# Optimization experiments

Hardware: AMD Instinct MI355X
Metric: run time of the kernel (lower is better)

## Reference

```python
import jax, jax.numpy as jnp
import numpy as np

DIM = 256
N_HEADS = 4
B, N = 2, 4096


def setup_inputs() -> dict:
    key = jax.random.key(0)
    ks = jax.random.split(key, 10)
    s = DIM ** -0.5
    return {
        "x": jax.random.normal(ks[0], (B, N, DIM), dtype=jnp.float32),
        "q_w": jax.random.normal(ks[1], (DIM, DIM), dtype=jnp.float32) * s,
        "q_b": jnp.zeros((DIM,), dtype=jnp.float32),
        "k_w": jax.random.normal(ks[2], (DIM, DIM), dtype=jnp.float32) * s,
        "k_b": jnp.zeros((DIM,), dtype=jnp.float32),
        "v_w": jax.random.normal(ks[3], (DIM, DIM), dtype=jnp.float32) * s,
        "v_b": jnp.zeros((DIM,), dtype=jnp.float32),
        "o_w": jax.random.normal(ks[4], (DIM, DIM), dtype=jnp.float32) * s,
        "o_b": jnp.zeros((DIM,), dtype=jnp.float32),
        "tau": jnp.ones((1,), dtype=jnp.float32),
    }


def reference(x, q_w, q_b, k_w, k_b, v_w, v_b, o_w, o_b, tau):
    Bsz, Nlen, C = x.shape
    H = N_HEADS
    Dh = C // H
    scale = C ** -0.5  # source uses full dim, not head_dim
    Q = (x @ q_w.T + q_b).reshape(Bsz, Nlen, H, Dh)
    K = (x @ k_w.T + k_b).reshape(Bsz, Nlen, H, Dh)
    V = (x @ v_w.T + v_b).reshape(Bsz, Nlen, H, Dh)
    attn = jnp.einsum('bnhd,bmhd->bhnm', Q, K) * scale
    # soft-threshold gate: keep only |attn| > tau, then relu
    attn = jax.nn.relu(jnp.where(jnp.abs(attn) > tau, attn, 0.0))
    attn = jax.nn.softmax(attn, axis=-1)
    out = jnp.einsum('bhnm,bmhd->bnhd', attn, V).reshape(Bsz, Nlen, C)
    return out @ o_w.T + o_b
```

## Files before the change

### kernel.cpp

```cpp
#include <hip/hip_runtime.h>

#define SEQ   4096
#define CDIM  256
#define NHEAD 4
#define DHEAD 64
#define PSTRIDE 72
#define LOG2E 1.4426950408889634f

typedef float    f32x4 __attribute__((ext_vector_type(4)));
typedef _Float16 f16x8 __attribute__((ext_vector_type(8)));
typedef _Float16 f16x4 __attribute__((ext_vector_type(4)));
typedef _Float16 f16x2 __attribute__((ext_vector_type(2)));

__device__ __forceinline__ f16x8 cvt_frag(const float* __restrict__ p) {
    float4 f0 = *(const float4*)p;
    float4 f1 = *(const float4*)(p + 4);
    f16x8 r;
    r[0]=(_Float16)f0.x; r[1]=(_Float16)f0.y; r[2]=(_Float16)f0.z; r[3]=(_Float16)f0.w;
    r[4]=(_Float16)f1.x; r[5]=(_Float16)f1.y; r[6]=(_Float16)f1.z; r[7]=(_Float16)f1.w;
    return r;
}

__device__ __forceinline__ f16x2 pkrtz(float a, float b) {
    return __builtin_bit_cast(f16x2, __builtin_amdgcn_cvt_pkrtz(a, b));
}

__global__ __launch_bounds__(256) void sta_prep(
    const float* __restrict__ qw, const float* __restrict__ kw,
    const float* __restrict__ vw, const float* __restrict__ ow,
    _Float16* __restrict__ w16)
{
    const int mat = blockIdx.y;
    const float* src = (mat == 0) ? qw : (mat == 1) ? kw : (mat == 2) ? vw : ow;
    const int i = (blockIdx.x * 256 + threadIdx.x) * 8;
    *(f16x8*)(w16 + mat * 65536 + i) = cvt_frag(src + i);
}

__global__ __launch_bounds__(256) void sta_qkv(
    const float* __restrict__ x, const _Float16* __restrict__ w16,
    const float* __restrict__ qb, const float* __restrict__ kb, const float* __restrict__ vb,
    _Float16* __restrict__ Qo, _Float16* __restrict__ Ko, _Float16* __restrict__ Vo)
{
    const int wave = threadIdx.x >> 6;
    const int lane = threadIdx.x & 63;
    const int l15  = lane & 15;
    const int quad = lane >> 4;
    const int mat  = blockIdx.y;
    const int half = blockIdx.z;
    const int row0 = blockIdx.x * 64 + wave * 16;

    const _Float16* w    = w16 + mat * 65536;
    const float*    bias = (mat == 0) ? qb : (mat == 1) ? kb : vb;

    f16x8 xf[8];
    const float* xrow = x + (row0 + l15) * CDIM + quad * 8;
    #pragma unroll
    for (int ks = 0; ks < 8; ks++) xf[ks] = cvt_frag(xrow + ks * 32);

    #pragma unroll 1
    for (int ct = 0; ct < 8; ct++) {
        const int ctg = half * 8 + ct;
        const _Float16* wr = w + (ctg * 16 + l15) * CDIM + quad * 8;
        f32x4 acc = {0.f, 0.f, 0.f, 0.f};
        if (mat < 2) {
            #pragma unroll
            for (int ks = 0; ks < 8; ks++)
                acc = __builtin_amdgcn_mfma_f32_16x16x32_f16(*(const f16x8*)(wr + ks * 32), xf[ks], acc, 0, 0, 0);
            const float4 bv = *(const float4*)(bias + ctg * 16 + quad * 4);
            const int c0 = ctg * 16 + quad * 4;
            const int h = c0 >> 6, d0 = c0 & 63;
            const int grow = row0 + l15, b = grow >> 12, n = grow & (SEQ - 1);
            const float sc = (mat == 0) ? (0.0625f * LOG2E) : 1.0f;
            f16x4 o;
            o[0] = (_Float16)((acc[0] + bv.x) * sc);
            o[1] = (_Float16)((acc[1] + bv.y) * sc);
            o[2] = (_Float16)((acc[2] + bv.z) * sc);
            o[3] = (_Float16)((acc[3] + bv.w) * sc);
            _Float16* dst = ((mat == 0) ? Qo : Ko) + (((b * NHEAD + h) * SEQ + n) * DHEAD + d0);
            *(f16x4*)dst = o;
        } else {
            #pragma unroll
            for (int ks = 0; ks < 8; ks++)
                acc = __builtin_amdgcn_mfma_f32_16x16x32_f16(xf[ks], *(const f16x8*)(wr + ks * 32), acc, 0, 0, 0);
            const int c = ctg * 16 + l15;
            const int h = c >> 6, d = c & 63;
            const float bv = bias[c];
            const int grow0 = row0 + quad * 4, b = grow0 >> 12, n0 = grow0 & (SEQ - 1);
            f16x4 o;
            #pragma unroll
            for (int r = 0; r < 4; r++) o[r] = (_Float16)(acc[r] + bv);
            *(f16x4*)(Vo + (((b * NHEAD + h) * DHEAD + d) * SEQ + n0)) = o;
        }
    }
}

__global__ __launch_bounds__(64) void sta_attn(
    const _Float16* __restrict__ Q, const _Float16* __restrict__ K, const _Float16* __restrict__ Vt,
    const float* __restrict__ taup,
    float* __restrict__ Opart, float* __restrict__ lpart)
{
    __shared__ __align__(16) _Float16 pbuf[2 * 64 * PSTRIDE];

    const int lane = threadIdx.x;
    const int l15  = lane & 15;
    const int quad = lane >> 4;
    const int qt = blockIdx.x;
    const int bh = blockIdx.y;
    const int sp = blockIdx.z;
    const float tau2 = __builtin_bit_cast(float, __builtin_amdgcn_readfirstlane(
        __builtin_bit_cast(int, fmaxf(taup[0], 0.0f) * LOG2E)));

    const _Float16* Qb = Q  + bh * SEQ * DHEAD;
    const _Float16* Kb = K  + bh * SEQ * DHEAD;
    const _Float16* Vb = Vt + bh * DHEAD * SEQ;

    const int q0 = qt * 64;

    _Float16* pw0 = pbuf + l15 * PSTRIDE + quad * 4;
    const _Float16* pr0 = pbuf + l15 * PSTRIDE + quad * 8;
    _Float16* pw1 = pw0 + 64 * PSTRIDE;
    const _Float16* pr1 = pr0 + 64 * PSTRIDE;
    const _Float16* Krow = Kb + l15 * DHEAD + quad * 8;

    f16x8 qf[4][2];
    #pragma unroll
    for (int qb = 0; qb < 4; qb++)
        #pragma unroll
        for (int ks = 0; ks < 2; ks++)
            qf[qb][ks] = *(const f16x8*)(Qb + (q0 + qb * 16 + l15) * DHEAD + ks * 32 + quad * 8);

    f32x4 O[4][4];
    #pragma unroll
    for (int qb = 0; qb < 4; qb++)
        #pragma unroll
        for (int db = 0; db < 4; db++) O[qb][db] = (f32x4){0.f, 0.f, 0.f, 0.f};
    float rs[4] = {0.f, 0.f, 0.f, 0.f};

    auto tile = [&](int kv0, _Float16* pw, const _Float16* pr) {
        const _Float16* Kt = Krow + kv0 * DHEAD;
        #pragma unroll
        for (int kb = 0; kb < 4; kb++) {
            f16x8 k0 = *(const f16x8*)(Kt + kb * 16 * DHEAD);
            f16x8 k1 = *(const f16x8*)(Kt + kb * 16 * DHEAD + 32);
            #pragma unroll
            for (int qb = 0; qb < 4; qb++) {
                f32x4 a = {0.f, 0.f, 0.f, 0.f};
                a = __builtin_amdgcn_mfma_f32_16x16x32_f16(k0, qf[qb][0], a, 0, 0, 0);
                a = __builtin_amdgcn_mfma_f32_16x16x32_f16(k1, qf[qb][1], a, 0, 0, 0);
                float p0 = (a[0] > tau2) ? __builtin_amdgcn_exp2f(a[0]) : 1.0f;
                float p1 = (a[1] > tau2) ? __builtin_amdgcn_exp2f(a[1]) : 1.0f;
                float p2 = (a[2] > tau2) ? __builtin_amdgcn_exp2f(a[2]) : 1.0f;
                float p3 = (a[3] > tau2) ? __builtin_amdgcn_exp2f(a[3]) : 1.0f;
                rs[qb] += (p0 + p1) + (p2 + p3);
                f16x2 lo = pkrtz(p0, p1);
                f16x2 hi = pkrtz(p2, p3);
                f16x4 pk;
                pk[0] = lo[0]; pk[1] = lo[1]; pk[2] = hi[0]; pk[3] = hi[1];
                *(f16x4*)(pw + qb * 16 * PSTRIDE + kb * 16) = pk;
            }
        }
        #pragma unroll
        for (int ks = 0; ks < 2; ks++) {
            f16x8 pa[4];
            #pragma unroll
            for (int qb = 0; qb < 4; qb++)
                pa[qb] = *(const f16x8*)(pr + qb * 16 * PSTRIDE + ks * 32);
            #pragma unroll
            for (int db = 0; db < 4; db++) {
                f16x8 vf = *(const f16x8*)(Vb + (db * 16 + l15) * SEQ + kv0 + ks * 32 + quad * 8);
                #pragma unroll
                for (int qb = 0; qb < 4; qb++)
                    O[qb][db] = __builtin_amdgcn_mfma_f32_16x16x32_f16(pa[qb], vf, O[qb][db], 0, 0, 0);
            }
        }
    };

    const int kvb = sp * 16 * 64;
    #pragma unroll 1
    for (int kp = 0; kp < 8; kp++) {
        tile(kvb + (kp * 2 + 0) * 64, pw0, pr0);
        tile(kvb + (kp * 2 + 1) * 64, pw1, pr1);
    }

    #pragma unroll
    for (int qb = 0; qb < 4; qb++) {
        float v = rs[qb];
        v += __shfl_xor(v, 16);
        v += __shfl_xor(v, 32);
        rs[qb] = v;
    }
    float* Ob = Opart + (size_t)((sp * 8 + bh) * SEQ + q0) * DHEAD;
    #pragma unroll
    for (int qb = 0; qb < 4; qb++)
        #pragma unroll
        for (int db = 0; db < 4; db++)
            #pragma unroll
            for (int r = 0; r < 4; r++)
                Ob[(qb * 16 + quad * 4 + r) * DHEAD + db * 16 + l15] = O[qb][db][r];
    if (quad == 0) {
        #pragma unroll
        for (int qb = 0; qb < 4; qb++)
            lpart[(sp * 8 + bh) * SEQ + q0 + qb * 16 + l15] = rs[qb];
    }
}

__global__ __launch_bounds__(128) void sta_oproj2(
    const float* __restrict__ Opart, const float* __restrict__ lpart,
    const _Float16* __restrict__ w16o, const float* __restrict__ ob,
    float* __restrict__ out)
{
    const int wave = threadIdx.x >> 6;
    const int lane = threadIdx.x & 63;
    const int l15  = lane & 15;
    const int quad = lane >> 4;
    const int row0 = blockIdx.x * 32 + wave * 16;
    const int half = blockIdx.y;

    const int nglob = row0 + l15;
    const int b = nglob >> 12, n = nglob & (SEQ - 1);

    f16x8 af[8];
    #pragma unroll
    for (int h = 0; h < 4; h++) {
        const int bhh = b * NHEAD + h;
        float lsum = 0.f;
        #pragma unroll
        for (int s = 0; s < 4; s++) lsum += lpart[(s * 8 + bhh) * SEQ + n];
        const float inv = 1.0f / lsum;
        #pragma unroll
        for (int dp = 0; dp < 2; dp++) {
            const int dh0 = dp * 32 + quad * 8;
            float a0x=0.f,a0y=0.f,a0z=0.f,a0w=0.f,a1x=0.f,a1y=0.f,a1z=0.f,a1w=0.f;
            #pragma unroll
            for (int s = 0; s < 4; s++) {
                const float* p = Opart + (size_t)((s * 8 + bhh) * SEQ + n) * DHEAD + dh0;
                const float4 t0 = *(const float4*)p;
                const float4 t1 = *(const float4*)(p + 4);
                a0x += t0.x; a0y += t0.y; a0z += t0.z; a0w += t0.w;
                a1x += t1.x; a1y += t1.y; a1z += t1.z; a1w += t1.w;
            }
            f16x8 v;
            v[0] = (_Float16)(a0x * inv); v[1] = (_Float16)(a0y * inv);
            v[2] = (_Float16)(a0z * inv); v[3] = (_Float16)(a0w * inv);
            v[4] = (_Float16)(a1x * inv); v[5] = (_Float16)(a1y * inv);
            v[6] = (_Float16)(a1z * inv); v[7] = (_Float16)(a1w * inv);
            af[h * 2 + dp] = v;
        }
    }

    #pragma unroll 1
    for (int ct = 0; ct < 8; ct++) {
        const int ctg = half * 8 + ct;
        const _Float16* wr = w16o + (ctg * 16 + l15) * CDIM + quad * 8;
        f32x4 acc = {0.f, 0.f, 0.f, 0.f};
        #pragma unroll
        for (int ks = 0; ks < 8; ks++)
            acc = __builtin_amdgcn_mfma_f32_16x16x32_f16(*(const f16x8*)(wr + ks * 32), af[ks], acc, 0, 0, 0);
        const int c0 = ctg * 16 + quad * 4;
        const float4 bv = *(const float4*)(ob + c0);
        float4 res;
        res.x = acc[0] + bv.x; res.y = acc[1] + bv.y;
        res.z = acc[2] + bv.z; res.w = acc[3] + bv.w;
        *(float4*)(out + (size_t)nglob * CDIM + c0) = res;
    }
}

extern "C" void kernel_launch(void* const* d_in, const int* in_sizes, int n_in,
                              void* d_out, int out_size, void* d_ws, size_t ws_size,
                              hipStream_t stream) {
    const float* x   = (const float*)d_in[0];
    const float* qw  = (const float*)d_in[1];
    const float* qb  = (const float*)d_in[2];
    const float* kw  = (const float*)d_in[3];
    const float* kb  = (const float*)d_in[4];
    const float* vw  = (const float*)d_in[5];
    const float* vb  = (const float*)d_in[6];
    const float* ow  = (const float*)d_in[7];
    const float* ob  = (const float*)d_in[8];
    const float* tau = (const float*)d_in[9];

    _Float16* w16 = (_Float16*)d_ws;
    _Float16* Q   = w16 + 262144;
    _Float16* K   = Q + 2097152;
    _Float16* Vt  = K + 2097152;
    float* Opart  = (float*)(Vt + 2097152);
    float* lpart  = Opart + 8388608;

    sta_prep  <<<dim3(32, 4),      256, 0, stream>>>(qw, kw, vw, ow, w16);
    sta_qkv   <<<dim3(128, 3, 2),  256, 0, stream>>>(x, w16, qb, kb, vb, Q, K, Vt);
    sta_attn  <<<dim3(64, 8, 4),    64, 0, stream>>>(Q, K, Vt, tau, Opart, lpart);
    sta_oproj2<<<dim3(256, 2),     128, 0, stream>>>(Opart, lpart, w16 + 3 * 65536, ob, (float*)d_out);
}
```

Baseline: 218.3 us.

## Software-pipeline attention loop: overlap QK/exp of next tile with PV of previous

After: 195.4 us. 10.5% less time.

```diff
diff --git a/kernel.cpp b/kernel.cpp
--- a/kernel.cpp
+++ b/kernel.cpp
@@ -116,11 +116,10 @@
 
     const int q0 = qt * 64;
 
-    _Float16* pw0 = pbuf + l15 * PSTRIDE + quad * 4;
-    const _Float16* pr0 = pbuf + l15 * PSTRIDE + quad * 8;
-    _Float16* pw1 = pw0 + 64 * PSTRIDE;
-    const _Float16* pr1 = pr0 + 64 * PSTRIDE;
+    _Float16* pw_base = pbuf + l15 * PSTRIDE + quad * 4;
+    const _Float16* pr_base = pbuf + l15 * PSTRIDE + quad * 8;
     const _Float16* Krow = Kb + l15 * DHEAD + quad * 8;
+    const _Float16* Vrow = Vb + l15 * SEQ + quad * 8;
 
     f16x8 qf[4][2];
     #pragma unroll
@@ -136,8 +135,10 @@
         for (int db = 0; db < 4; db++) O[qb][db] = (f32x4){0.f, 0.f, 0.f, 0.f};
     float rs[4] = {0.f, 0.f, 0.f, 0.f};
 
-    auto tile = [&](int kv0, _Float16* pw, const _Float16* pr) {
-        const _Float16* Kt = Krow + kv0 * DHEAD;
+    const int kt0 = sp * 16;
+
+    {
+        const _Float16* Kt = Krow + (kt0 * 64) * DHEAD;
         #pragma unroll
         for (int kb = 0; kb < 4; kb++) {
             f16x8 k0 = *(const f16x8*)(Kt + kb * 16 * DHEAD);
@@ -156,30 +157,73 @@
                 f16x2 hi = pkrtz(p2, p3);
                 f16x4 pk;
                 pk[0] = lo[0]; pk[1] = lo[1]; pk[2] = hi[0]; pk[3] = hi[1];
-                *(f16x4*)(pw + qb * 16 * PSTRIDE + kb * 16) = pk;
-            }
-        }
-        #pragma unroll
-        for (int ks = 0; ks < 2; ks++) {
-            f16x8 pa[4];
-            #pragma unroll
-            for (int qb = 0; qb < 4; qb++)
-                pa[qb] = *(const f16x8*)(pr + qb * 16 * PSTRIDE + ks * 32);
-            #pragma unroll
-            for (int db = 0; db < 4; db++) {
-                f16x8 vf = *(const f16x8*)(Vb + (db * 16 + l15) * SEQ + kv0 + ks * 32 + quad * 8);
+                *(f16x4*)(pw_base + qb * 16 * PSTRIDE + kb * 16) = pk;
+            }
+        }
+    }
+
+    #pragma unroll 1
+    for (int t = 1; t < 16; t++) {
+        const int kvc = (kt0 + t) * 64;
+        const int kvp = kvc - 64;
+        _Float16* pw = pw_base + (t & 1) * (64 * PSTRIDE);
+        const _Float16* pr = pr_base + ((t & 1) ^ 1) * (64 * PSTRIDE);
+        const _Float16* Kt = Krow + kvc * DHEAD;
+        f16x8 pa[4];
+        #pragma unroll
+        for (int c = 0; c < 4; c++) {
+            f16x8 k0 = *(const f16x8*)(Kt + c * 16 * DHEAD);
+            f16x8 k1 = *(const f16x8*)(Kt + c * 16 * DHEAD + 32);
+            #pragma unroll
+            for (int qb = 0; qb < 4; qb++) {
+                f32x4 a = {0.f, 0.f, 0.f, 0.f};
+                a = __builtin_amdgcn_mfma_f32_16x16x32_f16(k0, qf[qb][0], a, 0, 0, 0);
+                a = __builtin_amdgcn_mfma_f32_16x16x32_f16(k1, qf[qb][1], a, 0, 0, 0);
+                float p0 = (a[0] > tau2) ? __builtin_amdgcn_exp2f(a[0]) : 1.0f;
+                float p1 = (a[1] > tau2) ? __builtin_amdgcn_exp2f(a[1]) : 1.0f;
+                float p2 = (a[2] > tau2) ? __builtin_amdgcn_exp2f(a[2]) : 1.0f;
+                float p3 = (a[3] > tau2) ? __builtin_amdgcn_exp2f(a[3]) : 1.0f;
+                rs[qb] += (p0 + p1) + (p2 + p3);
+                f16x2 lo = pkrtz(p0, p1);
+                f16x2 hi = pkrtz(p2, p3);
+                f16x4 pk;
+                pk[0] = lo[0]; pk[1] = lo[1]; pk[2] = hi[0]; pk[3] = hi[1];
+                *(f16x4*)(pw + qb * 16 * PSTRIDE + c * 16) = pk;
+            }
+            const int ks = c >> 1, db0 = (c & 1) * 2;
+            if ((c & 1) == 0) {
+                #pragma unroll
+                for (int qb = 0; qb < 4; qb++)
+                    pa[qb] = *(const f16x8*)(pr + qb * 16 * PSTRIDE + ks * 32);
+            }
+            #pragma unroll
+            for (int dd = 0; dd < 2; dd++) {
+                const int db = db0 + dd;
+                f16x8 vf = *(const f16x8*)(Vrow + db * 16 * SEQ + kvp + ks * 32);
                 #pragma unroll
                 for (int qb = 0; qb < 4; qb++)
                     O[qb][db] = __builtin_amdgcn_mfma_f32_16x16x32_f16(pa[qb], vf, O[qb][db], 0, 0, 0);
             }
         }
-    };
-
-    const int kvb = sp * 16 * 64;
-    #pragma unroll 1
-    for (int kp = 0; kp < 8; kp++) {
-        tile(kvb + (kp * 2 + 0) * 64, pw0, pr0);
-        tile(kvb + (kp * 2 + 1) * 64, pw1, pr1);
+    }
+
+    {
+        const int kvp = (kt0 + 15) * 64;
+        const _Float16* pr = pr_base + (15 & 1) * (64 * PSTRIDE);
+        #pragma unroll
+        for (int ks = 0; ks < 2; ks++) {
+            f16x8 pa[4];
+            #pragma unroll
+            for (int qb = 0; qb < 4; qb++)
+                pa[qb] = *(const f16x8*)(pr + qb * 16 * PSTRIDE + ks * 32);
+            #pragma unroll
+            for (int db = 0; db < 4; db++) {
+                f16x8 vf = *(const f16x8*)(Vrow + db * 16 * SEQ + kvp + ks * 32);
+                #pragma unroll
+                for (int qb = 0; qb < 4; qb++)
+                    O[qb][db] = __builtin_amdgcn_mfma_f32_16x16x32_f16(pa[qb], vf, O[qb][db], 0, 0, 0);
+            }
+        }
     }
 
     #pragma unroll
```
